# Performance work log

Hardware: AMD Instinct MI355X
Metric: run time of the kernel (lower is better)

Reference implementation:

```python
import jax, jax.numpy as jnp
import numpy as np

ALPHA = 0.2  # LeakyReLU negative slope
NEG = -9e15


def gat_layer(h, adj, W, a):
    # Faithful to the torch GAT: e_ij = leakyrelu(a^T [Wh_i || Wh_j])
    # = leakyrelu(a_src . Wh_i + a_dst . Wh_j); avoids the NxNx2F materialization.
    Wh = h @ W                              # [N, F]
    Fo = W.shape[1]
    a_src, a_dst = a[:Fo, 0], a[Fo:, 0]
    e = jax.nn.leaky_relu(
        (Wh @ a_src)[:, None] + (Wh @ a_dst)[None, :], negative_slope=ALPHA
    )                                        # [N, N]
    e = jnp.where(adj > 0, e, NEG)
    att = jax.nn.softmax(e, axis=1)          # dropout p=0 (eval)
    return jax.nn.elu(att @ Wh)


def gru_cell(x, h, W_ih, W_hh, b_ih, b_hh):
    # PyTorch GRUCell semantics.
    gi = x @ W_ih.T + b_ih                   # [N, 3F]
    gh = h @ W_hh.T + b_hh
    i_r, i_z, i_n = jnp.split(gi, 3, axis=1)
    h_r, h_z, h_n = jnp.split(gh, 3, axis=1)
    r = jax.nn.sigmoid(i_r + h_r)
    z = jax.nn.sigmoid(i_z + h_z)
    n = jnp.tanh(i_n + r * h_n)
    return (1.0 - z) * n + z * h


def setup_inputs() -> dict:
    key = jax.random.key(0)
    ks = jax.random.split(key, 10)
    N, nfeat, nhid, nout = 8192, 256, 128, 128
    x = jax.random.normal(ks[0], (N, nfeat), dtype=jnp.float32)
    # sparse random binary adjacency (~32 avg degree) + self loops
    adj = (jax.random.uniform(ks[1], (N, N)) < 0.004).astype(jnp.float32)
    adj = jnp.maximum(adj, jnp.eye(N, dtype=jnp.float32))
    h_prev = jnp.zeros((N, nout), dtype=jnp.float32)

    def xavier(k, shape, gain=1.414):
        fan_in, fan_out = shape[0], shape[1]
        b = gain * np.sqrt(6.0 / (fan_in + fan_out))
        return jax.random.uniform(k, shape, jnp.float32, -b, b)

    W1 = xavier(ks[2], (nfeat, nhid))
    a1 = xavier(ks[3], (2 * nhid, 1))
    W2 = xavier(ks[4], (nhid, nout))
    a2 = xavier(ks[5], (2 * nout, 1))
    s = 1.0 / np.sqrt(nout)
    W_ih = jax.random.uniform(ks[6], (3 * nout, nout), jnp.float32, -s, s)
    W_hh = jax.random.uniform(ks[7], (3 * nout, nout), jnp.float32, -s, s)
    b_ih = jax.random.uniform(ks[8], (3 * nout,), jnp.float32, -s, s)
    b_hh = jax.random.uniform(ks[9], (3 * nout,), jnp.float32, -s, s)
    return {"x": x, "adj": adj, "h_prev": h_prev, "W1": W1, "a1": a1,
            "W2": W2, "a2": a2, "W_ih": W_ih, "W_hh": W_hh,
            "b_ih": b_ih, "b_hh": b_hh}


def reference(x, adj, h_prev, W1, a1, W2, a2, W_ih, W_hh, b_ih, b_hh):
    x1 = gat_layer(x, adj, W1, a1)
    h_spat = gat_layer(x1, adj, W2, a2)
    return gru_cell(h_spat, h_prev, W_ih, W_hh, b_ih, b_hh)
```

## Files before the change

kernel.cpp:

```cpp
#include <hip/hip_runtime.h>
#include <math.h>

#define N_NODES 8192
#define CAP 128
#define LRELU_ALPHA 0.2f

typedef float v4f __attribute__((ext_vector_type(4)));

template <int K>
__device__ __forceinline__ void gemm_from_lds(
    int r0, int t, const float* As, const float* __restrict__ W,
    const float* __restrict__ a, float* __restrict__ Wh, float* __restrict__ src,
    float* __restrict__ dst, float (*red)[4][2]) {
  int c = t & 127, half = t >> 7;
  float acc[4] = {0.f, 0.f, 0.f, 0.f};
  const float* Asl = As + (half * 4) * K;
#pragma unroll 8
  for (int k = 0; k < K; k++) {
    float wv = W[k * 128 + c];
#pragma unroll
    for (int r = 0; r < 4; r++) acc[r] += Asl[r * K + k] * wv;
  }
  float as = a[c], ad = a[128 + c];
  int wv_id = t >> 6, lane = t & 63;
#pragma unroll
  for (int r = 0; r < 4; r++) {
    int row = half * 4 + r;
    Wh[(size_t)(r0 + row) * 128 + c] = acc[r];
    float s = acc[r] * as, d = acc[r] * ad;
#pragma unroll
    for (int off = 32; off; off >>= 1) {
      s += __shfl_xor(s, off);
      d += __shfl_xor(d, off);
    }
    if (lane == 0) { red[wv_id][r][0] = s; red[wv_id][r][1] = d; }
  }
  __syncthreads();
  if (t < 8) {
    int wa = (t < 4) ? 0 : 2, rr = t & 3;
    src[r0 + t] = red[wa][rr][0] + red[wa + 1][rr][0];
    dst[r0 + t] = red[wa][rr][1] + red[wa + 1][rr][1];
  }
}

__device__ __forceinline__ void agg_pair(
    int i0, int s, int t, const float* __restrict__ Wh, const float* __restrict__ src,
    const float* __restrict__ dst, const int* __restrict__ idxbuf,
    const int* __restrict__ counts, float* tile, int (*jn)[128], float (*w)[128],
    float (*redm)[2], float (*reds)[2], float (*accs)[4][128]) {
  int half = t >> 7;
  int u = t & 127;
  int wv = (t >> 6) & 1;
  int i = i0 + s * 2 + half;
  int c = counts[i];
  float si = src[i];
  float e = -1e30f;
  if (u < c) {
    int j = idxbuf[(size_t)i * CAP + u];
    jn[half][u] = j;
    float xv = si + dst[j];
    e = xv > 0.f ? xv : LRELU_ALPHA * xv;
  }
  float m = e;
#pragma unroll
  for (int off = 32; off; off >>= 1) m = fmaxf(m, __shfl_xor(m, off));
  if ((t & 63) == 0) redm[half][wv] = m;
  __syncthreads();
  float M = fmaxf(redm[half][0], redm[half][1]);
  float ex = 0.f;
  if (u < c) {
    ex = expf(e - M);
    w[half][u] = ex;
  }
  float ss = ex;
#pragma unroll
  for (int off = 32; off; off >>= 1) ss += __shfl_xor(ss, off);
  if ((t & 63) == 0) reds[half][wv] = ss;
  __syncthreads();
  float inv = 1.f / (reds[half][0] + reds[half][1]);
  int slot = (t >> 5) & 3, col4 = t & 31;
  const float4* Wh4 = (const float4*)Wh;
  float ax = 0.f, ay = 0.f, az = 0.f, aw = 0.f;
  int k = slot;
  for (; k + 4 < c; k += 8) {
    float w0 = w[half][k], w1 = w[half][k + 4];
    float4 v0 = Wh4[(size_t)jn[half][k] * 32 + col4];
    float4 v1 = Wh4[(size_t)jn[half][k + 4] * 32 + col4];
    ax += w0 * v0.x + w1 * v1.x;
    ay += w0 * v0.y + w1 * v1.y;
    az += w0 * v0.z + w1 * v1.z;
    aw += w0 * v0.w + w1 * v1.w;
  }
  if (k < c) {
    float w0 = w[half][k];
    float4 v0 = Wh4[(size_t)jn[half][k] * 32 + col4];
    ax += w0 * v0.x; ay += w0 * v0.y; az += w0 * v0.z; aw += w0 * v0.w;
  }
  *(float4*)&accs[half][slot][col4 * 4] = make_float4(ax, ay, az, aw);
  __syncthreads();
  float r = accs[half][0][u] + accs[half][1][u] + accs[half][2][u] + accs[half][3][u];
  r *= inv;
  tile[(s * 2 + half) * 128 + u] = r > 0.f ? r : expf(r) - 1.f;
  __syncthreads();
}

__global__ __launch_bounds__(256) void kA(
    const float* __restrict__ adj, int* __restrict__ idxbuf, int* __restrict__ counts,
    const float* __restrict__ x, const float* __restrict__ W1, const float* __restrict__ a1,
    float* __restrict__ Wh1, float* __restrict__ src1, float* __restrict__ dst1,
    const float* __restrict__ Wi, const float* __restrict__ Whm, float* __restrict__ WiT,
    float* __restrict__ WhT) {
  __shared__ float As[8 * 256];
  __shared__ float red[4][4][2];
  __shared__ int jn[CAP];
  __shared__ int cnt;
  int t = threadIdx.x, b = blockIdx.x;
  if (b < N_NODES) {
    if (t == 0) cnt = 0;
    __syncthreads();
    const v4f* row = (const v4f*)(adj + (size_t)b * N_NODES);
    v4f v[8];
#pragma unroll
    for (int u = 0; u < 8; u++) v[u] = __builtin_nontemporal_load(row + t + 256 * u);
#pragma unroll
    for (int u = 0; u < 8; u++) {
      int n = (v[u].x > 0.f) + (v[u].y > 0.f) + (v[u].z > 0.f) + (v[u].w > 0.f);
      if (n) {
        int p = atomicAdd(&cnt, n);
        int j0 = (t + 256 * u) * 4;
        if (v[u].x > 0.f) { if (p < CAP) jn[p] = j0;     p++; }
        if (v[u].y > 0.f) { if (p < CAP) jn[p] = j0 + 1; p++; }
        if (v[u].z > 0.f) { if (p < CAP) jn[p] = j0 + 2; p++; }
        if (v[u].w > 0.f) { if (p < CAP) jn[p] = j0 + 3; p++; }
      }
    }
    __syncthreads();
    int c = cnt > CAP ? CAP : cnt;
    if (t < c) idxbuf[(size_t)b * CAP + t] = jn[t];
    if (t == 0) counts[b] = c;
  } else if (b < N_NODES + 1024) {
    int tile = b - N_NODES;
    const float4* Ab4 = (const float4*)(x + (size_t)tile * 8 * 256);
    float4* As4 = (float4*)As;
#pragma unroll
    for (int l = t; l < 8 * 256 / 4; l += 256) As4[l] = Ab4[l];
    __syncthreads();
    gemm_from_lds<256>(tile * 8, t, As, W1, a1, Wh1, src1, dst1, red);
  } else {
    for (int n = (b - N_NODES - 1024) * 256 + t; n < 384 * 128; n += 64 * 256) {
      int r = n >> 7, c = n & 127;
      WiT[c * 384 + r] = Wi[n];
      WhT[c * 384 + r] = Whm[n];
    }
  }
}

__global__ __launch_bounds__(256) void kB(
    const float* __restrict__ Wh1, const float* __restrict__ src1,
    const float* __restrict__ dst1, const int* __restrict__ idxbuf,
    const int* __restrict__ counts, const float* __restrict__ W2, const float* __restrict__ a2,
    float* __restrict__ Wh2, float* __restrict__ src2, float* __restrict__ dst2) {
  __shared__ float tile[8 * 128];
  __shared__ float red[4][4][2];
  __shared__ int jn[2][128];
  __shared__ float w[2][128];
  __shared__ float redm[2][2];
  __shared__ float reds[2][2];
  __shared__ float accs[2][4][128];
  int t = threadIdx.x, b = blockIdx.x;
  int i0 = b * 8;
#pragma unroll 1
  for (int s = 0; s < 4; s++)
    agg_pair(i0, s, t, Wh1, src1, dst1, idxbuf, counts, tile, jn, w, redm, reds, accs);
  gemm_from_lds<128>(i0, t, tile, W2, a2, Wh2, src2, dst2, red);
}

__global__ __launch_bounds__(256) void kC(
    const float* __restrict__ Wh2, const float* __restrict__ src2,
    const float* __restrict__ dst2, const int* __restrict__ idxbuf,
    const int* __restrict__ counts, const float* __restrict__ hprev,
    const float* __restrict__ WiT, const float* __restrict__ WhT,
    const float* __restrict__ b_ih, const float* __restrict__ b_hh, float* __restrict__ outp) {
  __shared__ float tile[8 * 128];
  __shared__ float hs[8 * 128];
  __shared__ int jn[2][128];
  __shared__ float w[2][128];
  __shared__ float redm[2][2];
  __shared__ float reds[2][2];
  __shared__ float accs[2][4][128];
  int t = threadIdx.x, b = blockIdx.x;
  int i0 = b * 8;
  ((float4*)hs)[t] = ((const float4*)(hprev + (size_t)i0 * 128))[t];
#pragma unroll 1
  for (int s = 0; s < 4; s++)
    agg_pair(i0, s, t, Wh2, src2, dst2, idxbuf, counts, tile, jn, w, redm, reds, accs);
  int c = t & 127, half = t >> 7;
  const float* xsl = tile + half * 4 * 128;
  const float* hsl = hs + half * 4 * 128;
  float rg[4], zg[4];
  {
    float ai[4] = {0.f}, ah[4] = {0.f};
#pragma unroll 4
    for (int k = 0; k < 128; k++) {
      float wi = WiT[k * 384 + c], wh = WhT[k * 384 + c];
#pragma unroll
      for (int r = 0; r < 4; r++) { ai[r] += xsl[r * 128 + k] * wi; ah[r] += hsl[r * 128 + k] * wh; }
    }
    float bi = b_ih[c], bh = b_hh[c];
#pragma unroll
    for (int r = 0; r < 4; r++) rg[r] = 1.f / (1.f + expf(-(ai[r] + bi + ah[r] + bh)));
  }
  {
    float ai[4] = {0.f}, ah[4] = {0.f};
#pragma unroll 4
    for (int k = 0; k < 128; k++) {
      float wi = WiT[k * 384 + 128 + c], wh = WhT[k * 384 + 128 + c];
#pragma unroll
      for (int r = 0; r < 4; r++) { ai[r] += xsl[r * 128 + k] * wi; ah[r] += hsl[r * 128 + k] * wh; }
    }
    float bi = b_ih[128 + c], bh = b_hh[128 + c];
#pragma unroll
    for (int r = 0; r < 4; r++) zg[r] = 1.f / (1.f + expf(-(ai[r] + bi + ah[r] + bh)));
  }
  {
    float ai[4] = {0.f}, ah[4] = {0.f};
#pragma unroll 4
    for (int k = 0; k < 128; k++) {
      float wi = WiT[k * 384 + 256 + c], wh = WhT[k * 384 + 256 + c];
#pragma unroll
      for (int r = 0; r < 4; r++) { ai[r] += xsl[r * 128 + k] * wi; ah[r] += hsl[r * 128 + k] * wh; }
    }
    float bi = b_ih[256 + c], bh = b_hh[256 + c];
#pragma unroll
    for (int r = 0; r < 4; r++) {
      float n = tanhf(ai[r] + bi + rg[r] * (ah[r] + bh));
      outp[(size_t)(i0 + half * 4 + r) * 128 + c] =
          (1.f - zg[r]) * n + zg[r] * hsl[r * 128 + c];
    }
  }
}

extern "C" void kernel_launch(void* const* d_in, const int* in_sizes, int n_in,
                              void* d_out, int out_size, void* d_ws, size_t ws_size,
                              hipStream_t stream) {
  const float* x     = (const float*)d_in[0];
  const float* adj   = (const float*)d_in[1];
  const float* hprev = (const float*)d_in[2];
  const float* W1    = (const float*)d_in[3];
  const float* a1    = (const float*)d_in[4];
  const float* W2    = (const float*)d_in[5];
  const float* a2    = (const float*)d_in[6];
  const float* Wi    = (const float*)d_in[7];
  const float* Whm   = (const float*)d_in[8];
  const float* b_ih  = (const float*)d_in[9];
  const float* b_hh  = (const float*)d_in[10];
  float* outp = (float*)d_out;

  char* p = (char*)d_ws;
  float* Wh1    = (float*)p; p += (size_t)N_NODES * 128 * 4;
  float* Wh2    = (float*)p; p += (size_t)N_NODES * 128 * 4;
  float* src1   = (float*)p; p += (size_t)N_NODES * 4;
  float* dst1   = (float*)p; p += (size_t)N_NODES * 4;
  float* src2   = (float*)p; p += (size_t)N_NODES * 4;
  float* dst2   = (float*)p; p += (size_t)N_NODES * 4;
  float* WiT    = (float*)p; p += (size_t)384 * 128 * 4;
  float* WhT    = (float*)p; p += (size_t)384 * 128 * 4;
  int*   counts = (int*)p;   p += (size_t)N_NODES * 4;
  int*   idxbuf = (int*)p;   p += (size_t)N_NODES * CAP * 4;

  kA<<<N_NODES + 1024 + 64, 256, 0, stream>>>(adj, idxbuf, counts, x, W1, a1, Wh1, src1, dst1,
                                              Wi, Whm, WiT, WhT);
  kB<<<N_NODES / 8, 256, 0, stream>>>(Wh1, src1, dst1, idxbuf, counts, W2, a2, Wh2, src2, dst2);
  kC<<<N_NODES / 8, 256, 0, stream>>>(Wh2, src2, dst2, idxbuf, counts, hprev, WiT, WhT, b_ih,
                                      b_hh, outp);
}
```

Before: 453.1 us.

## Aggregate each node with one wavefront using shuffles instead of block-wide LDS reductions

The sparse attention aggregation is restructured so that a single 64-lane wavefront handles one node. The softmax max and sum reductions are done entirely with wave shuffles, and neighbour indices and weights are broadcast via __shfl rather than staged through shared memory. This removes several __syncthreads per node pair and the LDS buffers for indices, weights and partial accumulators. In exchange, each lane reads float2 rows sequentially over the neighbours with less memory-level parallelism per node, though all four waves still work on different nodes concurrently.

```diff
diff --git a/kernel.cpp b/kernel.cpp
--- a/kernel.cpp
+++ b/kernel.cpp
@@ -43,65 +43,64 @@
   }
 }
 
-__device__ __forceinline__ void agg_pair(
-    int i0, int s, int t, const float* __restrict__ Wh, const float* __restrict__ src,
+__device__ __forceinline__ float2 agg_node_wave(
+    int i, int lane, const float* __restrict__ Wh, const float* __restrict__ src,
     const float* __restrict__ dst, const int* __restrict__ idxbuf,
-    const int* __restrict__ counts, float* tile, int (*jn)[128], float (*w)[128],
-    float (*redm)[2], float (*reds)[2], float (*accs)[4][128]) {
-  int half = t >> 7;
-  int u = t & 127;
-  int wv = (t >> 6) & 1;
-  int i = i0 + s * 2 + half;
+    const int* __restrict__ counts) {
   int c = counts[i];
   float si = src[i];
-  float e = -1e30f;
-  if (u < c) {
-    int j = idxbuf[(size_t)i * CAP + u];
-    jn[half][u] = j;
-    float xv = si + dst[j];
-    e = xv > 0.f ? xv : LRELU_ALPHA * xv;
-  }
-  float m = e;
+  int j0 = 0, j1 = 0;
+  float e0 = -1e30f, e1 = -1e30f;
+  if (lane < c) {
+    j0 = idxbuf[(size_t)i * CAP + lane];
+    float xv = si + dst[j0];
+    e0 = xv > 0.f ? xv : LRELU_ALPHA * xv;
+  }
+  if (lane + 64 < c) {
+    j1 = idxbuf[(size_t)i * CAP + lane + 64];
+    float xv = si + dst[j1];
+    e1 = xv > 0.f ? xv : LRELU_ALPHA * xv;
+  }
+  float m = fmaxf(e0, e1);
 #pragma unroll
   for (int off = 32; off; off >>= 1) m = fmaxf(m, __shfl_xor(m, off));
-  if ((t & 63) == 0) redm[half][wv] = m;
-  __syncthreads();
-  float M = fmaxf(redm[half][0], redm[half][1]);
-  float ex = 0.f;
-  if (u < c) {
-    ex = expf(e - M);
-    w[half][u] = ex;
-  }
-  float ss = ex;
-#pragma unroll
-  for (int off = 32; off; off >>= 1) ss += __shfl_xor(ss, off);
-  if ((t & 63) == 0) reds[half][wv] = ss;
-  __syncthreads();
-  float inv = 1.f / (reds[half][0] + reds[half][1]);
-  int slot = (t >> 5) & 3, col4 = t & 31;
-  const float4* Wh4 = (const float4*)Wh;
-  float ax = 0.f, ay = 0.f, az = 0.f, aw = 0.f;
-  int k = slot;
-  for (; k + 4 < c; k += 8) {
-    float w0 = w[half][k], w1 = w[half][k + 4];
-    float4 v0 = Wh4[(size_t)jn[half][k] * 32 + col4];
-    float4 v1 = Wh4[(size_t)jn[half][k + 4] * 32 + col4];
-    ax += w0 * v0.x + w1 * v1.x;
-    ay += w0 * v0.y + w1 * v1.y;
-    az += w0 * v0.z + w1 * v1.z;
-    aw += w0 * v0.w + w1 * v1.w;
-  }
-  if (k < c) {
-    float w0 = w[half][k];
-    float4 v0 = Wh4[(size_t)jn[half][k] * 32 + col4];
-    ax += w0 * v0.x; ay += w0 * v0.y; az += w0 * v0.z; aw += w0 * v0.w;
-  }
-  *(float4*)&accs[half][slot][col4 * 4] = make_float4(ax, ay, az, aw);
-  __syncthreads();
-  float r = accs[half][0][u] + accs[half][1][u] + accs[half][2][u] + accs[half][3][u];
-  r *= inv;
-  tile[(s * 2 + half) * 128 + u] = r > 0.f ? r : expf(r) - 1.f;
-  __syncthreads();
+  float w0 = (lane < c) ? expf(e0 - m) : 0.f;
+  float w1 = (lane + 64 < c) ? expf(e1 - m) : 0.f;
+  float s = w0 + w1;
+#pragma unroll
+  for (int off = 32; off; off >>= 1) s += __shfl_xor(s, off);
+  float inv = 1.f / s;
+  const float2* Wh2 = (const float2*)Wh;
+  float ax = 0.f, ay = 0.f;
+  int cc = c < 64 ? c : 64;
+  int k = 0;
+  for (; k + 3 < cc; k += 4) {
+    float wa = __shfl(w0, k),     wb = __shfl(w0, k + 1);
+    float wc_ = __shfl(w0, k + 2), wd = __shfl(w0, k + 3);
+    int ja = __shfl(j0, k),     jb = __shfl(j0, k + 1);
+    int jc = __shfl(j0, k + 2), jd = __shfl(j0, k + 3);
+    float2 va = Wh2[ja * 64 + lane];
+    float2 vb = Wh2[jb * 64 + lane];
+    float2 vc = Wh2[jc * 64 + lane];
+    float2 vd = Wh2[jd * 64 + lane];
+    ax += wa * va.x + wb * vb.x + wc_ * vc.x + wd * vd.x;
+    ay += wa * va.y + wb * vb.y + wc_ * vc.y + wd * vd.y;
+  }
+  for (; k < cc; k++) {
+    float wk = __shfl(w0, k);
+    int jk = __shfl(j0, k);
+    float2 v = Wh2[jk * 64 + lane];
+    ax += wk * v.x; ay += wk * v.y;
+  }
+  for (k = 64; k < c; k++) {
+    float wk = __shfl(w1, k - 64);
+    int jk = __shfl(j1, k - 64);
+    float2 v = Wh2[jk * 64 + lane];
+    ax += wk * v.x; ay += wk * v.y;
+  }
+  ax *= inv; ay *= inv;
+  return make_float2(ax > 0.f ? ax : expf(ax) - 1.f,
+                     ay > 0.f ? ay : expf(ay) - 1.f);
 }
 
 __global__ __launch_bounds__(256) void kA(
@@ -162,16 +161,14 @@
     float* __restrict__ Wh2, float* __restrict__ src2, float* __restrict__ dst2) {
   __shared__ float tile[8 * 128];
   __shared__ float red[4][4][2];
-  __shared__ int jn[2][128];
-  __shared__ float w[2][128];
-  __shared__ float redm[2][2];
-  __shared__ float reds[2][2];
-  __shared__ float accs[2][4][128];
   int t = threadIdx.x, b = blockIdx.x;
   int i0 = b * 8;
-#pragma unroll 1
-  for (int s = 0; s < 4; s++)
-    agg_pair(i0, s, t, Wh1, src1, dst1, idxbuf, counts, tile, jn, w, redm, reds, accs);
+  int wv = t >> 6, lane = t & 63;
+  float2 r0 = agg_node_wave(i0 + wv, lane, Wh1, src1, dst1, idxbuf, counts);
+  *(float2*)&tile[wv * 128 + 2 * lane] = r0;
+  float2 r1 = agg_node_wave(i0 + 4 + wv, lane, Wh1, src1, dst1, idxbuf, counts);
+  *(float2*)&tile[(4 + wv) * 128 + 2 * lane] = r1;
+  __syncthreads();
   gemm_from_lds<128>(i0, t, tile, W2, a2, Wh2, src2, dst2, red);
 }
 
@@ -183,17 +180,15 @@
     const float* __restrict__ b_ih, const float* __restrict__ b_hh, float* __restrict__ outp) {
   __shared__ float tile[8 * 128];
   __shared__ float hs[8 * 128];
-  __shared__ int jn[2][128];
-  __shared__ float w[2][128];
-  __shared__ float redm[2][2];
-  __shared__ float reds[2][2];
-  __shared__ float accs[2][4][128];
   int t = threadIdx.x, b = blockIdx.x;
   int i0 = b * 8;
   ((float4*)hs)[t] = ((const float4*)(hprev + (size_t)i0 * 128))[t];
-#pragma unroll 1
-  for (int s = 0; s < 4; s++)
-    agg_pair(i0, s, t, Wh2, src2, dst2, idxbuf, counts, tile, jn, w, redm, reds, accs);
+  int wv = t >> 6, lane = t & 63;
+  float2 r0 = agg_node_wave(i0 + wv, lane, Wh2, src2, dst2, idxbuf, counts);
+  *(float2*)&tile[wv * 128 + 2 * lane] = r0;
+  float2 r1 = agg_node_wave(i0 + 4 + wv, lane, Wh2, src2, dst2, idxbuf, counts);
+  *(float2*)&tile[(4 + wv) * 128 + 2 * lane] = r1;
+  __syncthreads();
   int c = t & 127, half = t >> 7;
   const float* xsl = tile + half * 4 * 128;
   const float* hsl = hs + half * 4 * 128;
```

After: 448.6 us. Within noise of the previous version (-1.0%).
